# Optimization experiments

Measured on AMD Instinct MI355X. Metric: run time of the kernel, lower is better.

## Reference

```python
import jax, jax.numpy as jnp
import numpy as np

HID = 1024
INTER = 4096
CLIP = 2.5          # config.clip_init_val; SymQuantizer clips to [-CLIP, CLIP]
W_BITS = 8
IN_BITS = 8
EPS = 1e-12         # BertLayerNorm eps


def sym_quant(x, clip, bits):
    """BiT SymQuantizer (layerwise): clamp, scale by global max-abs, round.
    STE: grads flow only through the clamp (zero outside [-clip, clip])."""
    n = float(2 ** (bits - 1) - 1)
    xc = jnp.clip(x, -clip, clip)
    m = jax.lax.stop_gradient(jnp.max(jnp.abs(xc)))
    s = n / m
    q = jnp.round(xc * s) / s
    return xc + jax.lax.stop_gradient(q - xc)


def setup_inputs() -> dict:
    key = jax.random.key(0)
    k0, k1, k2 = jax.random.split(key, 3)
    B, S = 4, 4096
    hidden_states = jax.random.normal(k0, (B, S, INTER), jnp.float32)
    input_tensor = jax.random.normal(k1, (B, S, HID), jnp.float32)
    W = jax.random.normal(k2, (HID, INTER), jnp.float32) * (1.0 / np.sqrt(INTER))
    b = jnp.zeros((HID,), jnp.float32)
    gamma = jnp.ones((HID,), jnp.float32)
    beta = jnp.zeros((HID,), jnp.float32)
    return {"hidden_states": hidden_states, "input_tensor": input_tensor,
            "W": W, "b": b, "gamma": gamma, "beta": beta}


def reference(hidden_states, input_tensor, W, b, gamma, beta):
    # QuantizeLinear: quantize weight and activation, then F.linear
    Wq = sym_quant(W, CLIP, W_BITS)          # [HID, INTER]
    xq = sym_quant(hidden_states, CLIP, IN_BITS)  # [B, S, INTER]
    h = jnp.einsum('bsi,oi->bso', xq, Wq) + b     # [B, S, HID]
    # dropout(p=0.0 / eval mode) is identity
    y = h + input_tensor
    # BertLayerNorm, eps=1e-12
    mu = jnp.mean(y, axis=-1, keepdims=True)
    var = jnp.mean((y - mu) ** 2, axis=-1, keepdims=True)
    return gamma * (y - mu) / jnp.sqrt(var + EPS) + beta
```

## Files before the change

kernel.cpp:

```cpp
#include <hip/hip_runtime.h>
#include <stdint.h>

#define MTOT  16384
#define KDIM  4096
#define NDIM  1024
#define CLIPV 2.5f
#define BK    64
#define NSTEP (KDIM / BK)

typedef __attribute__((ext_vector_type(4)))  int i32x4;
typedef __attribute__((ext_vector_type(16))) int i32x16;
typedef __attribute__((address_space(3))) void lvoid;
typedef __attribute__((address_space(1))) void gvoid;

#define G2L16(g, l) __builtin_amdgcn_global_load_lds((gvoid*)(g), (lvoid*)(l), 16, 0, 0)

__global__ __launch_bounds__(256) void maxabs_kernel(
    const float4* __restrict__ x, int n4, unsigned* __restrict__ slot) {
  __shared__ float red[4];
  float m = 0.f;
  const int stride = gridDim.x * blockDim.x;
  for (int i = blockIdx.x * blockDim.x + threadIdx.x; i < n4; i += stride) {
    float4 v = x[i];
    m = fmaxf(m, fmaxf(fmaxf(fabsf(v.x), fabsf(v.y)),
                       fmaxf(fabsf(v.z), fabsf(v.w))));
    if (__any(m >= CLIPV)) break;
  }
  m = fminf(m, CLIPV);
#pragma unroll
  for (int off = 32; off > 0; off >>= 1) m = fmaxf(m, __shfl_xor(m, off));
  if ((threadIdx.x & 63) == 0) red[threadIdx.x >> 6] = m;
  __syncthreads();
  if (threadIdx.x == 0) {
    float bm = fmaxf(fmaxf(red[0], red[1]), fmaxf(red[2], red[3]));
    atomicMax(slot, __float_as_uint(bm));
  }
}

__global__ __launch_bounds__(256) void quant_kernel(
    const float4* __restrict__ x, uint4* __restrict__ q, int n16,
    const unsigned* __restrict__ slot) {
  const float m = fminf(__uint_as_float(*slot), CLIPV);
  const float s = 127.0f / m;
  const int stride = gridDim.x * blockDim.x;
  for (int i = blockIdx.x * blockDim.x + threadIdx.x; i < n16; i += stride) {
    const float4* xp = x + 4 * (long)i;
    uint4 o;
    unsigned* op = (unsigned*)&o;
#pragma unroll
    for (int j = 0; j < 4; ++j) {
      float4 v = xp[j];
      int a = (int)rintf(fminf(fmaxf(v.x, -CLIPV), CLIPV) * s);
      int b = (int)rintf(fminf(fmaxf(v.y, -CLIPV), CLIPV) * s);
      int c = (int)rintf(fminf(fmaxf(v.z, -CLIPV), CLIPV) * s);
      int d = (int)rintf(fminf(fmaxf(v.w, -CLIPV), CLIPV) * s);
      op[j] = (unsigned)(a & 255) | ((unsigned)(b & 255) << 8) |
              ((unsigned)(c & 255) << 16) | ((unsigned)(d & 255) << 24);
    }
    q[i] = o;
  }
}

__global__ __launch_bounds__(256, 2) void gemm_i8(
    const int8_t* __restrict__ qA, const int8_t* __restrict__ qB,
    float* __restrict__ out, const float* __restrict__ resid,
    const float* __restrict__ bias,
    const unsigned* __restrict__ slot_x, const unsigned* __restrict__ slot_w) {
  __shared__ __align__(16) int8_t As[2][128 * BK];
  __shared__ __align__(16) int8_t Bs[2][256 * BK];

  const int t  = threadIdx.x;
  const int l  = t & 63;
  const int w  = t >> 6;
  const int wm = (w & 1) * 64;
  const int wn = (w >> 1) * 128;
  const int lr = l & 31;
  const int lh = l >> 5;

  const long m0 = (long)blockIdx.y * 128;
  const long n0 = (long)blockIdx.x * 256;

  i32x16 acc[2][4] = {};

  const int8_t* gA[2];
  const int8_t* gB[4];
#pragma unroll
  for (int j = 0; j < 2; ++j) {
    const int s = t + 256 * j, row = s >> 2, cc = (s & 3) ^ ((row >> 1) & 3);
    gA[j] = qA + (m0 + row) * KDIM + cc * 16;
  }
#pragma unroll
  for (int j = 0; j < 4; ++j) {
    const int s = t + 256 * j, row = s >> 2, cc = (s & 3) ^ ((row >> 1) & 3);
    gB[j] = qB + (n0 + row) * KDIM + cc * 16;
  }
  const int ldsb = (t & 192) * 16;

  int abase[2], amask[2], bbase[4], bmask[4];
#pragma unroll
  for (int mt = 0; mt < 2; ++mt) {
    const int ra = wm + mt * 32 + lr;
    abase[mt] = ra * BK; amask[mt] = (ra >> 1) & 3;
  }
#pragma unroll
  for (int nt = 0; nt < 4; ++nt) {
    const int rb = wn + nt * 32 + lr;
    bbase[nt] = rb * BK; bmask[nt] = (rb >> 1) & 3;
  }

#define STAGE(buf, koff)                                      \
  do {                                                        \
    _Pragma("unroll")                                         \
    for (int j = 0; j < 2; ++j)                               \
      G2L16(gA[j] + (koff), &As[buf][ldsb + j * 4096]);       \
    _Pragma("unroll")                                         \
    for (int j = 0; j < 4; ++j)                               \
      G2L16(gB[j] + (koff), &Bs[buf][ldsb + j * 4096]);       \
  } while (0)

  STAGE(0, 0);

#pragma unroll 2
  for (int ks = 0; ks < NSTEP; ++ks) {
    const int cur = ks & 1;
    if (ks + 1 < NSTEP) {
      STAGE(cur ^ 1, (ks + 1) * BK);
      asm volatile("s_waitcnt vmcnt(6)" ::: "memory");
    } else {
      asm volatile("s_waitcnt vmcnt(0)" ::: "memory");
    }
    __builtin_amdgcn_s_barrier();
    asm volatile("" ::: "memory");

    const int8_t* A_ = As[cur];
    const int8_t* B_ = Bs[cur];
#pragma unroll
    for (int kk = 0; kk < 2; ++kk) {
      const int c = kk * 2 + lh;
      i32x4 a0 = *(const i32x4*)(A_ + abase[0] + ((c ^ amask[0]) << 4));
      i32x4 a1 = *(const i32x4*)(A_ + abase[1] + ((c ^ amask[1]) << 4));
      i32x4 b0 = *(const i32x4*)(B_ + bbase[0] + ((c ^ bmask[0]) << 4));
      i32x4 b1 = *(const i32x4*)(B_ + bbase[1] + ((c ^ bmask[1]) << 4));
      i32x4 b2 = *(const i32x4*)(B_ + bbase[2] + ((c ^ bmask[2]) << 4));
      i32x4 b3 = *(const i32x4*)(B_ + bbase[3] + ((c ^ bmask[3]) << 4));
      acc[0][0] = __builtin_amdgcn_mfma_i32_32x32x32_i8(a0, b0, acc[0][0], 0, 0, 0);
      acc[1][0] = __builtin_amdgcn_mfma_i32_32x32x32_i8(a1, b0, acc[1][0], 0, 0, 0);
      acc[0][1] = __builtin_amdgcn_mfma_i32_32x32x32_i8(a0, b1, acc[0][1], 0, 0, 0);
      acc[1][1] = __builtin_amdgcn_mfma_i32_32x32x32_i8(a1, b1, acc[1][1], 0, 0, 0);
      acc[0][2] = __builtin_amdgcn_mfma_i32_32x32x32_i8(a0, b2, acc[0][2], 0, 0, 0);
      acc[1][2] = __builtin_amdgcn_mfma_i32_32x32x32_i8(a1, b2, acc[1][2], 0, 0, 0);
      acc[0][3] = __builtin_amdgcn_mfma_i32_32x32x32_i8(a0, b3, acc[0][3], 0, 0, 0);
      acc[1][3] = __builtin_amdgcn_mfma_i32_32x32x32_i8(a1, b3, acc[1][3], 0, 0, 0);
    }
    asm volatile("s_waitcnt lgkmcnt(0)" ::: "memory");
    __builtin_amdgcn_s_barrier();
    asm volatile("" ::: "memory");
  }
#undef STAGE

  const float mx = fminf(__uint_as_float(*slot_x), CLIPV);
  const float mw = fminf(__uint_as_float(*slot_w), CLIPV);
  const float S  = mx * mw * (1.0f / (127.0f * 127.0f));

  const int coln = (int)n0 + wn + lr;
  float bv[4];
#pragma unroll
  for (int nt = 0; nt < 4; ++nt) bv[nt] = bias[coln + nt * 32];

#pragma unroll
  for (int mt = 0; mt < 2; ++mt)
#pragma unroll
    for (int r = 0; r < 16; ++r) {
      const long row = m0 + wm + mt * 32 + (r & 3) + 8 * (r >> 2) + 4 * lh;
      float* orow = out + row * NDIM + coln;
      const float* rrow = resid + row * NDIM + coln;
#pragma unroll
      for (int nt = 0; nt < 4; ++nt)
        orow[nt * 32] = (float)acc[mt][nt][r] * S + bv[nt] + rrow[nt * 32];
    }
}

__global__ __launch_bounds__(256) void ln_kernel(
    float* __restrict__ h, const float* __restrict__ gamma,
    const float* __restrict__ beta) {
  const int lane = threadIdx.x & 63;
  const long row = (long)blockIdx.x * 4 + (threadIdx.x >> 6);
  float4* hp = (float4*)(h + row * NDIM);
  float4 y[4];
  float sum = 0.f, ss = 0.f;
#pragma unroll
  for (int j = 0; j < 4; ++j) {
    y[j] = hp[lane + 64 * j];
    sum += y[j].x + y[j].y + y[j].z + y[j].w;
    ss  += y[j].x * y[j].x + y[j].y * y[j].y + y[j].z * y[j].z + y[j].w * y[j].w;
  }
#pragma unroll
  for (int off = 32; off > 0; off >>= 1) {
    sum += __shfl_xor(sum, off);
    ss  += __shfl_xor(ss, off);
  }
  const float mu   = sum * (1.0f / NDIM);
  const float var  = ss * (1.0f / NDIM) - mu * mu;
  const float rstd = rsqrtf(var + 1e-12f);
#pragma unroll
  for (int j = 0; j < 4; ++j) {
    float4 g  = ((const float4*)gamma)[lane + 64 * j];
    float4 be = ((const float4*)beta)[lane + 64 * j];
    float4 o;
    o.x = g.x * (y[j].x - mu) * rstd + be.x;
    o.y = g.y * (y[j].y - mu) * rstd + be.y;
    o.z = g.z * (y[j].z - mu) * rstd + be.z;
    o.w = g.w * (y[j].w - mu) * rstd + be.w;
    hp[lane + 64 * j] = o;
  }
}

extern "C" void kernel_launch(void* const* d_in, const int* in_sizes, int n_in,
                              void* d_out, int out_size, void* d_ws,
                              size_t ws_size, hipStream_t stream) {
  const float* x     = (const float*)d_in[0];
  const float* resid = (const float*)d_in[1];
  const float* W     = (const float*)d_in[2];
  const float* b     = (const float*)d_in[3];
  const float* gamma = (const float*)d_in[4];
  const float* beta  = (const float*)d_in[5];
  float* out = (float*)d_out;

  int8_t* qA = (int8_t*)d_ws;
  int8_t* qW = qA + (size_t)MTOT * KDIM;
  unsigned* slots = (unsigned*)(qW + (size_t)NDIM * KDIM);

  hipMemsetAsync(slots, 0, 8, stream);
  maxabs_kernel<<<2048, 256, 0, stream>>>((const float4*)x, MTOT * KDIM / 4, slots);
  maxabs_kernel<<<512, 256, 0, stream>>>((const float4*)W, NDIM * KDIM / 4, slots + 1);
  quant_kernel<<<2048, 256, 0, stream>>>((const float4*)x, (uint4*)qA,
                                         MTOT * KDIM / 16, slots);
  quant_kernel<<<512, 256, 0, stream>>>((const float4*)W, (uint4*)qW,
                                        NDIM * KDIM / 16, slots + 1);
  gemm_i8<<<dim3(NDIM / 256, MTOT / 128), 256, 0, stream>>>(qA, qW, out, resid, b,
                                                            slots, slots + 1);
  ln_kernel<<<MTOT / 4, 256, 0, stream>>>(out, gamma, beta);
}
```

Measured before the change: 572.2 us.

## Replace double-buffered BK=64 pipeline with single-buffer BK=128 and block remap

Removes the double-buffered LDS staging with manual vmcnt waits and uses one LDS buffer at a K-tile of 128, with a full-row XOR swizzle of 8 chunks. Each iteration loads the tile, syncs, computes, and syncs again, so loads no longer overlap with MFMA work inside a block. It also remaps the block index so consecutive blocks walk along M for a fixed N tile, which may improve L2 reuse of the weight tile. Loss of intra-block overlap is offset only by other resident blocks hiding latency.

```diff
diff --git a/kernel.cpp b/kernel.cpp
--- a/kernel.cpp
+++ b/kernel.cpp
@@ -5,8 +5,6 @@
 #define KDIM  4096
 #define NDIM  1024
 #define CLIPV 2.5f
-#define BK    64
-#define NSTEP (KDIM / BK)
 
 typedef __attribute__((ext_vector_type(4)))  int i32x4;
 typedef __attribute__((ext_vector_type(16))) int i32x16;
@@ -66,8 +64,8 @@
     float* __restrict__ out, const float* __restrict__ resid,
     const float* __restrict__ bias,
     const unsigned* __restrict__ slot_x, const unsigned* __restrict__ slot_w) {
-  __shared__ __align__(16) int8_t As[2][128 * BK];
-  __shared__ __align__(16) int8_t Bs[2][256 * BK];
+  __shared__ __align__(16) int8_t As[128 * 128];
+  __shared__ __align__(16) int8_t Bs[256 * 128];
 
   const int t  = threadIdx.x;
   const int l  = t & 63;
@@ -77,21 +75,22 @@
   const int lr = l & 31;
   const int lh = l >> 5;
 
-  const long m0 = (long)blockIdx.y * 128;
-  const long n0 = (long)blockIdx.x * 256;
+  const int b = blockIdx.x + 4 * blockIdx.y;
+  const long m0 = (long)(b & 127) * 128;
+  const long n0 = (long)(b >> 7) * 256;
 
   i32x16 acc[2][4] = {};
 
-  const int8_t* gA[2];
-  const int8_t* gB[4];
-#pragma unroll
-  for (int j = 0; j < 2; ++j) {
-    const int s = t + 256 * j, row = s >> 2, cc = (s & 3) ^ ((row >> 1) & 3);
+  const int8_t* gA[4];
+  const int8_t* gB[8];
+#pragma unroll
+  for (int j = 0; j < 4; ++j) {
+    const int s = t + 256 * j, row = s >> 3, cc = (s & 7) ^ (row & 7);
     gA[j] = qA + (m0 + row) * KDIM + cc * 16;
   }
 #pragma unroll
-  for (int j = 0; j < 4; ++j) {
-    const int s = t + 256 * j, row = s >> 2, cc = (s & 3) ^ ((row >> 1) & 3);
+  for (int j = 0; j < 8; ++j) {
+    const int s = t + 256 * j, row = s >> 3, cc = (s & 7) ^ (row & 7);
     gB[j] = qB + (n0 + row) * KDIM + cc * 16;
   }
   const int ldsb = (t & 192) * 16;
@@ -100,49 +99,29 @@
 #pragma unroll
   for (int mt = 0; mt < 2; ++mt) {
     const int ra = wm + mt * 32 + lr;
-    abase[mt] = ra * BK; amask[mt] = (ra >> 1) & 3;
+    abase[mt] = ra * 128; amask[mt] = ra & 7;
   }
 #pragma unroll
   for (int nt = 0; nt < 4; ++nt) {
     const int rb = wn + nt * 32 + lr;
-    bbase[nt] = rb * BK; bmask[nt] = (rb >> 1) & 3;
-  }
-
-#define STAGE(buf, koff)                                      \
-  do {                                                        \
-    _Pragma("unroll")                                         \
-    for (int j = 0; j < 2; ++j)                               \
-      G2L16(gA[j] + (koff), &As[buf][ldsb + j * 4096]);       \
-    _Pragma("unroll")                                         \
-    for (int j = 0; j < 4; ++j)                               \
-      G2L16(gB[j] + (koff), &Bs[buf][ldsb + j * 4096]);       \
-  } while (0)
-
-  STAGE(0, 0);
-
-#pragma unroll 2
-  for (int ks = 0; ks < NSTEP; ++ks) {
-    const int cur = ks & 1;
-    if (ks + 1 < NSTEP) {
-      STAGE(cur ^ 1, (ks + 1) * BK);
-      asm volatile("s_waitcnt vmcnt(6)" ::: "memory");
-    } else {
-      asm volatile("s_waitcnt vmcnt(0)" ::: "memory");
-    }
-    __builtin_amdgcn_s_barrier();
-    asm volatile("" ::: "memory");
-
-    const int8_t* A_ = As[cur];
-    const int8_t* B_ = Bs[cur];
-#pragma unroll
-    for (int kk = 0; kk < 2; ++kk) {
+    bbase[nt] = rb * 128; bmask[nt] = rb & 7;
+  }
+
+  for (int k0 = 0; k0 < KDIM; k0 += 128) {
+#pragma unroll
+    for (int j = 0; j < 4; ++j) G2L16(gA[j] + k0, As + ldsb + j * 4096);
+#pragma unroll
+    for (int j = 0; j < 8; ++j) G2L16(gB[j] + k0, Bs + ldsb + j * 4096);
+    __syncthreads();
+#pragma unroll
+    for (int kk = 0; kk < 4; ++kk) {
       const int c = kk * 2 + lh;
-      i32x4 a0 = *(const i32x4*)(A_ + abase[0] + ((c ^ amask[0]) << 4));
-      i32x4 a1 = *(const i32x4*)(A_ + abase[1] + ((c ^ amask[1]) << 4));
-      i32x4 b0 = *(const i32x4*)(B_ + bbase[0] + ((c ^ bmask[0]) << 4));
-      i32x4 b1 = *(const i32x4*)(B_ + bbase[1] + ((c ^ bmask[1]) << 4));
-      i32x4 b2 = *(const i32x4*)(B_ + bbase[2] + ((c ^ bmask[2]) << 4));
-      i32x4 b3 = *(const i32x4*)(B_ + bbase[3] + ((c ^ bmask[3]) << 4));
+      i32x4 a0 = *(const i32x4*)(As + abase[0] + ((c ^ amask[0]) << 4));
+      i32x4 a1 = *(const i32x4*)(As + abase[1] + ((c ^ amask[1]) << 4));
+      i32x4 b0 = *(const i32x4*)(Bs + bbase[0] + ((c ^ bmask[0]) << 4));
+      i32x4 b1 = *(const i32x4*)(Bs + bbase[1] + ((c ^ bmask[1]) << 4));
+      i32x4 b2 = *(const i32x4*)(Bs + bbase[2] + ((c ^ bmask[2]) << 4));
+      i32x4 b3 = *(const i32x4*)(Bs + bbase[3] + ((c ^ bmask[3]) << 4));
       acc[0][0] = __builtin_amdgcn_mfma_i32_32x32x32_i8(a0, b0, acc[0][0], 0, 0, 0);
       acc[1][0] = __builtin_amdgcn_mfma_i32_32x32x32_i8(a1, b0, acc[1][0], 0, 0, 0);
       acc[0][1] = __builtin_amdgcn_mfma_i32_32x32x32_i8(a0, b1, acc[0][1], 0, 0, 0);
@@ -152,11 +131,8 @@
       acc[0][3] = __builtin_amdgcn_mfma_i32_32x32x32_i8(a0, b3, acc[0][3], 0, 0, 0);
       acc[1][3] = __builtin_amdgcn_mfma_i32_32x32x32_i8(a1, b3, acc[1][3], 0, 0, 0);
     }
-    asm volatile("s_waitcnt lgkmcnt(0)" ::: "memory");
-    __builtin_amdgcn_s_barrier();
-    asm volatile("" ::: "memory");
-  }
-#undef STAGE
+    __syncthreads();
+  }
 
   const float mx = fminf(__uint_as_float(*slot_x), CLIPV);
   const float mw = fminf(__uint_as_float(*slot_w), CLIPV);
```

After: 561.8 us. Within noise of the previous version (-1.8%).

## Fuse LayerNorm into int8 GEMM epilogue with full-row 64x1024 tiles

Applied to the files above, without the earlier changes.

Replaces the 128x256-tile GEMM and the separate LayerNorm kernel with one kernel. Each 512-thread block computes a 64-row by 1024-column output tile, so an entire hidden row is resident and the mean and variance can be reduced through shuffles and shared memory. This removes the write and re-read of the intermediate output and one kernel launch. In exchange, each block restreams the whole weight matrix, uses about 136KB of dynamic shared memory, and runs with only one block per CU.

```diff
diff --git a/kernel.cpp b/kernel.cpp
--- a/kernel.cpp
+++ b/kernel.cpp
@@ -8,8 +8,9 @@
 #define BK    64
 #define NSTEP (KDIM / BK)
 
-typedef __attribute__((ext_vector_type(4)))  int i32x4;
-typedef __attribute__((ext_vector_type(16))) int i32x16;
+typedef __attribute__((ext_vector_type(4)))  int   i32x4;
+typedef __attribute__((ext_vector_type(16))) int   i32x16;
+typedef __attribute__((ext_vector_type(16))) float f32x16;
 typedef __attribute__((address_space(3))) void lvoid;
 typedef __attribute__((address_space(1))) void gvoid;
 
@@ -61,61 +62,56 @@
   }
 }
 
-__global__ __launch_bounds__(256, 2) void gemm_i8(
+__global__ __launch_bounds__(512, 1) void gemm_ln(
     const int8_t* __restrict__ qA, const int8_t* __restrict__ qB,
     float* __restrict__ out, const float* __restrict__ resid,
-    const float* __restrict__ bias,
+    const float* __restrict__ bias, const float* __restrict__ gamma,
+    const float* __restrict__ beta,
     const unsigned* __restrict__ slot_x, const unsigned* __restrict__ slot_w) {
-  __shared__ __align__(16) int8_t As[2][128 * BK];
-  __shared__ __align__(16) int8_t Bs[2][256 * BK];
+  extern __shared__ __align__(16) int8_t smem[];
+  int8_t* const As0 = smem;
+  int8_t* const Bs0 = smem + 8192;
 
   const int t  = threadIdx.x;
   const int l  = t & 63;
   const int w  = t >> 6;
-  const int wm = (w & 1) * 64;
-  const int wn = (w >> 1) * 128;
   const int lr = l & 31;
   const int lh = l >> 5;
 
-  const long m0 = (long)blockIdx.y * 128;
-  const long n0 = (long)blockIdx.x * 256;
+  const long m0 = (long)blockIdx.x * 64;
 
   i32x16 acc[2][4] = {};
 
-  const int8_t* gA[2];
-  const int8_t* gB[4];
-#pragma unroll
-  for (int j = 0; j < 2; ++j) {
-    const int s = t + 256 * j, row = s >> 2, cc = (s & 3) ^ ((row >> 1) & 3);
-    gA[j] = qA + (m0 + row) * KDIM + cc * 16;
-  }
-#pragma unroll
-  for (int j = 0; j < 4; ++j) {
-    const int s = t + 256 * j, row = s >> 2, cc = (s & 3) ^ ((row >> 1) & 3);
-    gB[j] = qB + (n0 + row) * KDIM + cc * 16;
-  }
-  const int ldsb = (t & 192) * 16;
+  const int8_t* gAp = qA;
+  if (w < 4) {
+    const int s = w * 64 + l, row = s >> 2, cc = (s & 3) ^ ((row >> 1) & 3);
+    gAp = qA + (m0 + row) * KDIM + cc * 16;
+  }
+  const int8_t* gBp[8];
+#pragma unroll
+  for (int j = 0; j < 8; ++j) {
+    const int s = (j * 8 + w) * 64 + l, row = s >> 2, cc = (s & 3) ^ ((row >> 1) & 3);
+    gBp[j] = qB + (long)row * KDIM + cc * 16;
+  }
 
   int abase[2], amask[2], bbase[4], bmask[4];
 #pragma unroll
   for (int mt = 0; mt < 2; ++mt) {
-    const int ra = wm + mt * 32 + lr;
+    const int ra = mt * 32 + lr;
     abase[mt] = ra * BK; amask[mt] = (ra >> 1) & 3;
   }
 #pragma unroll
   for (int nt = 0; nt < 4; ++nt) {
-    const int rb = wn + nt * 32 + lr;
+    const int rb = w * 128 + nt * 32 + lr;
     bbase[nt] = rb * BK; bmask[nt] = (rb >> 1) & 3;
   }
 
-#define STAGE(buf, koff)                                      \
-  do {                                                        \
-    _Pragma("unroll")                                         \
-    for (int j = 0; j < 2; ++j)                               \
-      G2L16(gA[j] + (koff), &As[buf][ldsb + j * 4096]);       \
-    _Pragma("unroll")                                         \
-    for (int j = 0; j < 4; ++j)                               \
-      G2L16(gB[j] + (koff), &Bs[buf][ldsb + j * 4096]);       \
+#define STAGE(buf, koff)                                                  \
+  do {                                                                    \
+    if (w < 4) G2L16(gAp + (koff), As0 + (buf) * 4096 + w * 1024);        \
+    _Pragma("unroll")                                                     \
+    for (int j = 0; j < 8; ++j)                                           \
+      G2L16(gBp[j] + (koff), Bs0 + (buf) * 65536 + (j * 8 + w) * 1024);   \
   } while (0)
 
   STAGE(0, 0);
@@ -125,15 +121,15 @@
     const int cur = ks & 1;
     if (ks + 1 < NSTEP) {
       STAGE(cur ^ 1, (ks + 1) * BK);
-      asm volatile("s_waitcnt vmcnt(6)" ::: "memory");
+      asm volatile("s_waitcnt vmcnt(8)" ::: "memory");
     } else {
       asm volatile("s_waitcnt vmcnt(0)" ::: "memory");
     }
     __builtin_amdgcn_s_barrier();
     asm volatile("" ::: "memory");
 
-    const int8_t* A_ = As[cur];
-    const int8_t* B_ = Bs[cur];
+    const int8_t* A_ = As0 + cur * 4096;
+    const int8_t* B_ = Bs0 + cur * 65536;
 #pragma unroll
     for (int kk = 0; kk < 2; ++kk) {
       const int c = kk * 2 + lh;
@@ -162,57 +158,67 @@
   const float mw = fminf(__uint_as_float(*slot_w), CLIPV);
   const float S  = mx * mw * (1.0f / (127.0f * 127.0f));
 
-  const int coln = (int)n0 + wn + lr;
-  float bv[4];
-#pragma unroll
-  for (int nt = 0; nt < 4; ++nt) bv[nt] = bias[coln + nt * 32];
-
+  const int coln = w * 128 + lr;
+  float bia[4], gam[4], bet[4];
+#pragma unroll
+  for (int nt = 0; nt < 4; ++nt) {
+    bia[nt] = bias[coln + nt * 32];
+    gam[nt] = gamma[coln + nt * 32];
+    bet[nt] = beta[coln + nt * 32];
+  }
+
+  f32x16 yf[2][4];
 #pragma unroll
   for (int mt = 0; mt < 2; ++mt)
 #pragma unroll
+    for (int nt = 0; nt < 4; ++nt)
+#pragma unroll
+      for (int r = 0; r < 16; ++r) {
+        const int lrow = mt * 32 + (r & 3) + 8 * (r >> 2) + 4 * lh;
+        yf[mt][nt][r] = (float)acc[mt][nt][r] * S + bia[nt]
+                      + resid[(m0 + lrow) * NDIM + coln + nt * 32];
+      }
+
+  float* red = (float*)smem;
+#pragma unroll
+  for (int mt = 0; mt < 2; ++mt)
+#pragma unroll
     for (int r = 0; r < 16; ++r) {
-      const long row = m0 + wm + mt * 32 + (r & 3) + 8 * (r >> 2) + 4 * lh;
-      float* orow = out + row * NDIM + coln;
-      const float* rrow = resid + row * NDIM + coln;
+      const int lrow = mt * 32 + (r & 3) + 8 * (r >> 2) + 4 * lh;
+      float s1 = 0.f, s2 = 0.f;
+#pragma unroll
+      for (int nt = 0; nt < 4; ++nt) {
+        const float v = yf[mt][nt][r];
+        s1 += v; s2 += v * v;
+      }
+#pragma unroll
+      for (int off = 16; off > 0; off >>= 1) {
+        s1 += __shfl_xor(s1, off);
+        s2 += __shfl_xor(s2, off);
+      }
+      if (lr == 0) { red[lrow * 16 + w * 2] = s1; red[lrow * 16 + w * 2 + 1] = s2; }
+    }
+  __syncthreads();
+
+#pragma unroll
+  for (int mt = 0; mt < 2; ++mt)
+#pragma unroll
+    for (int r = 0; r < 16; ++r) {
+      const int lrow = mt * 32 + (r & 3) + 8 * (r >> 2) + 4 * lh;
+      float s1 = 0.f, s2 = 0.f;
+#pragma unroll
+      for (int g = 0; g < 8; ++g) {
+        s1 += red[lrow * 16 + g * 2];
+        s2 += red[lrow * 16 + g * 2 + 1];
+      }
+      const float mu   = s1 * (1.0f / NDIM);
+      const float var  = s2 * (1.0f / NDIM) - mu * mu;
+      const float rstd = rsqrtf(var + 1e-12f);
+      float* orow = out + (m0 + lrow) * NDIM + coln;
 #pragma unroll
       for (int nt = 0; nt < 4; ++nt)
-        orow[nt * 32] = (float)acc[mt][nt][r] * S + bv[nt] + rrow[nt * 32];
-    }
-}
-
-__global__ __launch_bounds__(256) void ln_kernel(
-    float* __restrict__ h, const float* __restrict__ gamma,
-    const float* __restrict__ beta) {
-  const int lane = threadIdx.x & 63;
-  const long row = (long)blockIdx.x * 4 + (threadIdx.x >> 6);
-  float4* hp = (float4*)(h + row * NDIM);
-  float4 y[4];
-  float sum = 0.f, ss = 0.f;
-#pragma unroll
-  for (int j = 0; j < 4; ++j) {
-    y[j] = hp[lane + 64 * j];
-    sum += y[j].x + y[j].y + y[j].z + y[j].w;
-    ss  += y[j].x * y[j].x + y[j].y * y[j].y + y[j].z * y[j].z + y[j].w * y[j].w;
-  }
-#pragma unroll
-  for (int off = 32; off > 0; off >>= 1) {
-    sum += __shfl_xor(sum, off);
-    ss  += __shfl_xor(ss, off);
-  }
-  const float mu   = sum * (1.0f / NDIM);
-  const float var  = ss * (1.0f / NDIM) - mu * mu;
-  const float rstd = rsqrtf(var + 1e-12f);
-#pragma unroll
-  for (int j = 0; j < 4; ++j) {
-    float4 g  = ((const float4*)gamma)[lane + 64 * j];
-    float4 be = ((const float4*)beta)[lane + 64 * j];
-    float4 o;
-    o.x = g.x * (y[j].x - mu) * rstd + be.x;
-    o.y = g.y * (y[j].y - mu) * rstd + be.y;
-    o.z = g.z * (y[j].z - mu) * rstd + be.z;
-    o.w = g.w * (y[j].w - mu) * rstd + be.w;
-    hp[lane + 64 * j] = o;
-  }
+        orow[nt * 32] = gam[nt] * (yf[mt][nt][r] - mu) * rstd + bet[nt];
+    }
 }
 
 extern "C" void kernel_launch(void* const* d_in, const int* in_sizes, int n_in,
@@ -237,7 +243,6 @@
                                          MTOT * KDIM / 16, slots);
   quant_kernel<<<512, 256, 0, stream>>>((const float4*)W, (uint4*)qW,
                                         NDIM * KDIM / 16, slots + 1);
-  gemm_i8<<<dim3(NDIM / 256, MTOT / 128), 256, 0, stream>>>(qA, qW, out, resid, b,
-                                                            slots, slots + 1);
-  ln_kernel<<<MTOT / 4, 256, 0, stream>>>(out, gamma, beta);
-}
+  gemm_ln<<<MTOT / 64, 512, 2 * 4096 + 2 * 65536, stream>>>(
+      qA, qW, out, resid, b, gamma, beta, slots, slots + 1);
+}
```

New measurement: 628.2 us. 9.8% more time.
